# Kernel optimization log

Hardware: AMD Instinct MI355X
Metric: run time of the kernel (lower is better)

The kernel has to match this reference:

```python
import jax, jax.numpy as jnp
import numpy as np

EPS = 1e-5

def knn_idx(x, k):
    # x: (B,C,N). Returns (B,N,k) indices of k nearest neighbors (by L2).
    inner = -2.0 * jnp.einsum('bcn,bcm->bnm', x, x)          # (B,N,N)
    xx = jnp.sum(x * x, axis=1)                               # (B,N)
    neg_dist = -xx[:, :, None] - inner - xx[:, None, :]       # (B,N,N)
    _, idx = jax.lax.top_k(neg_dist, k)                       # (B,N,k)
    return idx

def get_graph_features(x, k):
    # x: (B,C,N) -> (B,2C,N,k) with channels = concat(neighbor-center, center)
    B, C, N = x.shape
    idx = knn_idx(x, k)                                       # (B,N,k)
    pts = jnp.transpose(x, (0, 2, 1))                         # (B,N,C)
    nbr = jax.vmap(lambda p, i: p[i])(pts, idx)               # (B,N,k,C)
    ctr = jnp.broadcast_to(pts[:, :, None, :], nbr.shape)     # (B,N,k,C)
    feat = jnp.concatenate([nbr - ctr, ctr], axis=-1)         # (B,N,k,2C)
    return jnp.transpose(feat, (0, 3, 1, 2))                  # (B,2C,N,k)

def conv_bn_relu(y, W, gamma, beta):
    # 1x1 conv (pointwise matmul) + train-mode BatchNorm2d + ReLU
    y = jnp.einsum('oc,bcnk->bonk', W, y)
    mean = jnp.mean(y, axis=(0, 2, 3), keepdims=True)
    var = jnp.var(y, axis=(0, 2, 3), keepdims=True)
    yhat = (y - mean) * jax.lax.rsqrt(var + EPS)
    return jax.nn.relu(yhat * gamma[None, :, None, None] + beta[None, :, None, None])

def setup_inputs() -> dict:
    key = jax.random.key(0)
    ks = jax.random.split(key, 16)
    B, N, k, emb = 8, 2048, 20, 512
    x = jax.random.normal(ks[0], (B, 3, N), dtype=jnp.float32)
    def w(kk, o, c):
        return jax.random.normal(kk, (o, c), dtype=jnp.float32) * (1.0 / np.sqrt(c))
    inp = {
        'x': x, 'k': k,
        'W1': w(ks[1], 64, 6),   'W2': w(ks[2], 64, 64),
        'W3': w(ks[3], 128, 64), 'W4': w(ks[4], 256, 128),
        'W5': w(ks[5], emb, 512),
    }
    for i, c in zip(range(1, 6), [64, 64, 128, 256, emb]):
        inp[f'g{i}'] = 1.0 + 0.1 * jax.random.normal(ks[5 + i], (c,), dtype=jnp.float32)
        inp[f'b{i}'] = 0.1 * jax.random.normal(ks[10 + i], (c,), dtype=jnp.float32)
    return inp

def reference(x, W1, W2, W3, W4, W5, g1, b1, g2, b2, g3, b3, g4, b4, g5, b5, k):
    B, C, N = x.shape
    h = get_graph_features(x, k)                  # (B,6,N,k)
    h = conv_bn_relu(h, W1, g1, b1)               # (B,64,N,k)
    x1 = jnp.max(h, axis=-1, keepdims=True)
    h = conv_bn_relu(h, W2, g2, b2)               # (B,64,N,k)
    x2 = jnp.max(h, axis=-1, keepdims=True)
    h = conv_bn_relu(h, W3, g3, b3)               # (B,128,N,k)
    x3 = jnp.max(h, axis=-1, keepdims=True)
    h = conv_bn_relu(h, W4, g4, b4)               # (B,256,N,k)
    x4 = jnp.max(h, axis=-1, keepdims=True)
    cat = jnp.concatenate([x1, x2, x3, x4], axis=1)  # (B,512,N,1)
    out = conv_bn_relu(cat, W5, g5, b5)              # (B,emb,N,1)
    return out.reshape(B, -1, N)
```

## Files before the change

kernel.cpp:

```cpp
#include <hip/hip_runtime.h>
#include <hip/hip_bf16.h>

typedef __hip_bfloat16 bf16;
typedef __attribute__((ext_vector_type(8))) short short8v;
typedef __attribute__((ext_vector_type(4))) float f32x4;
typedef unsigned int uint;
typedef unsigned long long u64;

#define BATCH 8
#define NPTS 2048
#define KNN 20
#define NK (NPTS*KNN)
#define P4 (BATCH*NK)
#define BN_TOT (BATCH*NPTS)

union BU { bf16 h; unsigned short u; };
__device__ __forceinline__ unsigned short f2bf(float f){
    BU bu; bu.h = __float2bfloat16(f); return bu.u;
}
__device__ __forceinline__ float bfu2f(unsigned short u){
    return __uint_as_float(((uint)u) << 16);
}
__device__ __forceinline__ uint fenc(float f){
    uint b = __float_as_uint(f);
    return (b & 0x80000000u) ? ~b : (b | 0x80000000u);
}

__global__ void initK(float* __restrict__ shadow)
{
    int t = blockIdx.x*256 + threadIdx.x;
    if (t < 5*16*1024) shadow[t] = 0.f;
}

__global__ void cvtWS(const float* __restrict__ src, short* __restrict__ dst, int Cin)
{
    int t = blockIdx.x*256 + threadIdx.x;
    int co = t / Cin, ci = t - co*Cin;
    dst[(size_t)co*Cin + (ci ^ ((co & 7) << 3))] = (short)f2bf(src[t]);
}

__global__ __launch_bounds__(512)
void knn_kernel(const float* __restrict__ x, int* __restrict__ idx)
{
    #pragma clang fp contract(off)
    __shared__ float4 sp[NPTS];
    const int b  = blockIdx.x / (NPTS/8);
    const int nb = blockIdx.x % (NPTS/8);
    const float* xb = x + (size_t)b*3*NPTS;
    for (int i = threadIdx.x; i < NPTS; i += 512) {
        float y0 = xb[i], y1 = xb[NPTS+i], y2 = xb[2*NPTS+i];
        float4 p; p.x = y0; p.y = y1; p.z = y2;
        p.w = y0*y0 + y1*y1 + y2*y2;
        sp[i] = p;
    }
    __syncthreads();

    const int wave = threadIdx.x >> 6;
    const int lane = threadIdx.x & 63;
    const int n = nb*8 + wave;

    const float4 pn = sp[n];
    const float x0 = pn.x, x1 = pn.y, x2 = pn.z;
    const float xxn = pn.w;

    constexpr int L = 4;
    float bA[L], bB[L]; int iA[L], iB[L];
    #pragma unroll
    for (int i = 0; i < L; ++i) {
        bA[i] = -3e38f; bB[i] = -3e38f; iA[i] = 0x7fffffff; iB[i] = 0x7fffffff;
    }

    float4 c0 = sp[lane], c1 = sp[lane + 64];
    #pragma unroll
    for (int t = 0; t < NPTS/128; ++t) {
        float4 n0, n1;
        if (t + 1 < NPTS/128) {
            n0 = sp[lane + (2*t+2)*64];
            n1 = sp[lane + (2*t+3)*64];
        }
        int m0 = lane + (2*t)*64, m1 = m0 + 64;
        float dot0 = x0*c0.x + x1*c0.y + x2*c0.z;
        float v0 = -xxn - (-2.f*dot0) - c0.w;
        float dot1 = x0*c1.x + x1*c1.y + x2*c1.z;
        float v1 = -xxn - (-2.f*dot1) - c1.w;
        int mi0 = m0, mi1 = m1;
        #pragma unroll
        for (int i = 0; i < L; ++i) {
            { bool sw = v0 > bA[i];
              float tv = sw ? bA[i] : v0; int ti = sw ? iA[i] : mi0;
              bA[i] = sw ? v0 : bA[i]; iA[i] = sw ? mi0 : iA[i]; v0 = tv; mi0 = ti; }
            { bool sw = v1 > bB[i];
              float tv = sw ? bB[i] : v1; int ti = sw ? iB[i] : mi1;
              bB[i] = sw ? v1 : bB[i]; iB[i] = sw ? mi1 : iB[i]; v1 = tv; mi1 = ti; }
        }
        c0 = n0; c1 = n1;
    }

    u64 kA[L], kB[L];
    #pragma unroll
    for (int i = 0; i < L; ++i) {
        kA[i] = ((u64)fenc(bA[i]) << 32) | (uint)(~iA[i]);
        kB[i] = ((u64)fenc(bB[i]) << 32) | (uint)(~iB[i]);
    }

    size_t obase = ((size_t)b*NPTS + n)*KNN;
    int popA = 0, popB = 0;
    #pragma unroll 1
    for (int s = 0; s < KNN; ++s) {
        bool useA = kA[0] >= kB[0];
        u64 my = useA ? kA[0] : kB[0];
        u64 g = my;
        #pragma unroll
        for (int off = 1; off < 64; off <<= 1) {
            u64 o = __shfl_xor(g, off);
            g = (o > g) ? o : g;
        }
        if (lane == 0) idx[obase + s] = (int)(~(uint)g);
        bool win = (my == g);
        bool pA = win && useA, pB = win && !useA;
        #pragma unroll
        for (int i = 0; i < L-1; ++i) {
            kA[i] = pA ? kA[i+1] : kA[i];
            kB[i] = pB ? kB[i+1] : kB[i];
        }
        kA[L-1] = pA ? 0ULL : kA[L-1];
        kB[L-1] = pB ? 0ULL : kB[L-1];
        popA += pA; popB += pB;
    }

    if (__any((popA >= L) || (popB >= L))) {
        float B[KNN]; int BI[KNN];
        #pragma unroll
        for (int i = 0; i < KNN; ++i) { B[i] = -3e38f; BI[i] = 0x7fffffff; }
        #pragma unroll 1
        for (int j = 0; j < NPTS/64; ++j) {
            int m = lane + j*64;
            float4 p = sp[m];
            float dot = x0*p.x + x1*p.y + x2*p.z;
            float v = -xxn - (-2.f*dot) - p.w;
            int mi = m;
            #pragma unroll
            for (int i = 0; i < KNN; ++i) {
                bool sw = v > B[i];
                float tv = sw ? B[i]  : v;
                int   ti = sw ? BI[i] : mi;
                B[i]  = sw ? v  : B[i];
                BI[i] = sw ? mi : BI[i];
                v = tv; mi = ti;
            }
        }
        #pragma unroll 1
        for (int s = 0; s < KNN; ++s) {
            float mv = B[0]; int mi = BI[0];
            #pragma unroll
            for (int off = 1; off < 64; off <<= 1) {
                float ov = __shfl_xor(mv, off);
                int   oi = __shfl_xor(mi, off);
                if (ov > mv || (ov == mv && oi < mi)) { mv = ov; mi = oi; }
            }
            bool win = (B[0] == mv) && (BI[0] == mi);
            #pragma unroll
            for (int i = 0; i < KNN-1; ++i) {
                B[i]  = win ? B[i+1]  : B[i];
                BI[i] = win ? BI[i+1] : BI[i];
            }
            B[KNN-1]  = win ? -3e38f     : B[KNN-1];
            BI[KNN-1] = win ? 0x7fffffff : BI[KNN-1];
            if (lane == 0) idx[obase + s] = mi;
        }
    }
}

__global__ __launch_bounds__(256)
void conv1T(const float* __restrict__ x, const int* __restrict__ idx,
            const float* __restrict__ W1, bf16* __restrict__ h1,
            float* __restrict__ shadow)
{
    __shared__ unsigned short lv[256][64];
    __shared__ float ps[4][64], pq[4][64];
    const int tid = threadIdx.x;
    int p = blockIdx.x*256 + tid;
    int b = p / NK;
    int r = p - b*NK;
    int n = r / KNN;
    int j = idx[p];
    const float* xb = x + (size_t)b*3*NPTS;
    float c0 = xb[n], c1 = xb[NPTS+n], c2 = xb[2*NPTS+n];
    float d0 = xb[j]-c0, d1 = xb[NPTS+j]-c1, d2 = xb[2*NPTS+j]-c2;
    uint4* outp = reinterpret_cast<uint4*>(reinterpret_cast<unsigned short*>(h1) + (size_t)p*64);
    uint4* lrow = reinterpret_cast<uint4*>(lv[tid]);
    #pragma unroll
    for (int ch = 0; ch < 8; ++ch) {
        uint u[4];
        #pragma unroll
        for (int q = 0; q < 4; ++q) {
            const float* wa = W1 + (ch*8 + q*2)*6;
            float a0 = wa[0]*d0 + wa[1]*d1 + wa[2]*d2 + wa[3]*c0 + wa[4]*c1 + wa[5]*c2;
            const float* wb = wa + 6;
            float a1 = wb[0]*d0 + wb[1]*d1 + wb[2]*d2 + wb[3]*c0 + wb[4]*c1 + wb[5]*c2;
            u[q] = (uint)f2bf(a0) | ((uint)f2bf(a1) << 16);
        }
        uint4 val = make_uint4(u[0], u[1], u[2], u[3]);
        outp[ch] = val;
        lrow[ch] = val;
    }
    __syncthreads();
    int c = tid & 63, grp = tid >> 6;
    float s = 0.f, q = 0.f;
    #pragma unroll 8
    for (int i = 0; i < 64; ++i) {
        float v = bfu2f(lv[grp*64 + i][c]);
        s += v; q += v*v;
    }
    ps[grp][c] = s; pq[grp][c] = q;
    __syncthreads();
    if (tid < 64) {
        float S = ps[0][tid]+ps[1][tid]+ps[2][tid]+ps[3][tid];
        float Q = pq[0][tid]+pq[1][tid]+pq[2][tid]+pq[3][tid];
        float* sh = shadow + (size_t)(blockIdx.x & 15)*1024;
        atomicAdd(&sh[tid], S);
        atomicAdd(&sh[512 + tid], Q);
    }
}

__global__ void fin_kernel(const float* __restrict__ shadow,
                           const float* __restrict__ gamma, const float* __restrict__ beta,
                           float* __restrict__ scbiF, int C, float invCnt)
{
    for (int c = threadIdx.x; c < C; c += 256) {
        float s = 0.f, q = 0.f;
        #pragma unroll
        for (int i = 0; i < 16; ++i) { s += shadow[i*1024 + c]; q += shadow[i*1024 + 512 + c]; }
        float m = s*invCnt;
        float var = q*invCnt - m*m;
        float rs = rsqrtf(var + 1e-5f);
        float sc = rs * gamma[c];
        float bi = fmaf(-m, sc, beta[c]);
        scbiF[2*c] = sc; scbiF[2*c+1] = bi;
    }
}

template<int Cout, int Cin, int M, int POOL, int NSPLIT, int KTILE, int BT, int PF>
__global__ __launch_bounds__(BT)
void gemmT(const short* __restrict__ Wb, const bf16* __restrict__ in,
           bf16* __restrict__ outT, float* __restrict__ shadow,
           float* __restrict__ pmax, float* __restrict__ pmin)
{
    constexpr int CSPL = Cout/NSPLIT;
    constexpr int NT   = CSPL/16;
    constexpr int ROWS = (BT/64)*16*M;
    constexpr int KSTOT = Cin/32;
    constexpr int KPT   = KTILE/32;
    constexpr int NTILE = Cin/KTILE;
    constexpr int NG    = POOL ? ROWS/KNN : 1;
    constexpr size_t WB = (size_t)CSPL*KTILE*2;
    constexpr size_t PB = POOL ? (size_t)2*ROWS*17*4 : 0;
    constexpr size_t SB = WB > PB ? WB : PB;

    __shared__ __align__(16) char smem[SB];
    short* WsmS = reinterpret_cast<short*>(smem);
    float* poolF = reinterpret_cast<float*>(smem);

    const int tid  = threadIdx.x;
    const int lane = tid & 63;
    const int g = lane >> 4, mr = lane & 15;
    const int wid = tid >> 6;
    const int rowBlk = blockIdx.x*ROWS;
    const int rowW   = rowBlk + wid*(16*M);
    const int ntBase = blockIdx.y*CSPL;
    const short* inS = reinterpret_cast<const short*>(in);

    f32x4 acc[M][NT];
    #pragma unroll
    for (int m = 0; m < M; ++m)
    #pragma unroll
    for (int i = 0; i < NT; ++i) acc[m][i] = (f32x4){0.f,0.f,0.f,0.f};

    if constexpr (PF == 2) {
        static_assert(NTILE == 1, "PF=2 requires KTILE==Cin");
        short8v aAll[M*KSTOT];
        #pragma unroll
        for (int ks = 0; ks < KSTOT; ++ks)
        #pragma unroll
        for (int m = 0; m < M; ++m)
            aAll[ks*M + m] = *reinterpret_cast<const short8v*>(
                inS + (size_t)(rowW + m*16 + mr)*Cin + ks*32 + 8*g);
        for (int f8 = tid; f8 < CSPL*KTILE/8; f8 += BT) {
            int f = f8*8;
            int row = f / KTILE, col = f - row*KTILE;
            short8v v = *reinterpret_cast<const short8v*>(
                Wb + (size_t)(ntBase + row)*Cin + col);
            *reinterpret_cast<short8v*>(WsmS + f) = v;
        }
        __syncthreads();
        #pragma unroll
        for (int ks = 0; ks < KSTOT; ++ks) {
            const int kx = ks*32 + 8*g;
            #pragma unroll
            for (int nt = 0; nt < NT; ++nt) {
                const int brow = nt*16 + mr;
                short8v bfr = *reinterpret_cast<const short8v*>(
                    WsmS + brow*KTILE + (kx ^ ((mr & 7) << 3)));
                #pragma unroll
                for (int m = 0; m < M; ++m)
                    acc[m][nt] = __builtin_amdgcn_mfma_f32_16x16x32_bf16(
                        aAll[ks*M + m], bfr, acc[m][nt], 0, 0, 0);
            }
        }
    } else {
        short8v a[M], anext[M];
        if (PF) {
            #pragma unroll
            for (int m = 0; m < M; ++m)
                a[m] = *reinterpret_cast<const short8v*>(inS + (size_t)(rowW + m*16 + mr)*Cin + 8*g);
        }
        #pragma unroll 1
        for (int kt = 0; kt < NTILE; ++kt) {
            if (kt) __syncthreads();
            {
                const int ktBase = kt*KTILE;
                for (int f8 = tid; f8 < CSPL*KTILE/8; f8 += BT) {
                    int f = f8*8;
                    int row = f / KTILE, col = f - row*KTILE;
                    short8v v = *reinterpret_cast<const short8v*>(
                        Wb + (size_t)(ntBase + row)*Cin + ktBase + col);
                    *reinterpret_cast<short8v*>(WsmS + f) = v;
                }
            }
            __syncthreads();

            #pragma unroll
            for (int ksl = 0; ksl < KPT; ++ksl) {
                const int ksg = kt*KPT + ksl;
                const int k0 = ksg*32 + 8*g;
                if (!PF) {
                    #pragma unroll
                    for (int m = 0; m < M; ++m)
                        a[m] = *reinterpret_cast<const short8v*>(inS + (size_t)(rowW + m*16 + mr)*Cin + k0);
                } else if (ksg + 1 < KSTOT) {
                    #pragma unroll
                    for (int m = 0; m < M; ++m)
                        anext[m] = *reinterpret_cast<const short8v*>(inS + (size_t)(rowW + m*16 + mr)*Cin + k0 + 32);
                }
                const int kx = ksl*32 + 8*g;
                #pragma unroll
                for (int nt = 0; nt < NT; ++nt) {
                    const int brow = nt*16 + mr;
                    short8v bfr = *reinterpret_cast<const short8v*>(
                        WsmS + brow*KTILE + (kx ^ ((mr & 7) << 3)));
                    #pragma unroll
                    for (int m = 0; m < M; ++m)
                        acc[m][nt] = __builtin_amdgcn_mfma_f32_16x16x32_bf16(a[m], bfr, acc[m][nt], 0, 0, 0);
                }
                if (PF) {
                    #pragma unroll
                    for (int m = 0; m < M; ++m) a[m] = anext[m];
                }
            }
        }
    }

    float* sh = shadow + (size_t)((blockIdx.x ^ blockIdx.y) & 15)*1024;
    #pragma unroll
    for (int nt = 0; nt < NT; ++nt) {
        float s = 0.f, q = 0.f;
        #pragma unroll
        for (int m = 0; m < M; ++m)
        #pragma unroll
        for (int j = 0; j < 4; ++j) { float v = acc[m][nt][j]; s += v; q += v*v; }
        s += __shfl_xor(s, 16); s += __shfl_xor(s, 32);
        q += __shfl_xor(q, 16); q += __shfl_xor(q, 32);
        if (g == 0) {
            atomicAdd(&sh[ntBase + nt*16 + mr], s);
            atomicAdd(&sh[512 + ntBase + nt*16 + mr], q);
        }
    }

    if (!POOL) {
        #pragma unroll
        for (int m = 0; m < M; ++m)
        #pragma unroll
        for (int nt = 0; nt < NT; ++nt)
        #pragma unroll
        for (int j = 0; j < 4; ++j) {
            size_t row = (size_t)rowW + m*16 + g*4 + j;
            outT[row*Cout + ntBase + nt*16 + mr] = __float2bfloat16(acc[m][nt][j]);
        }
    } else {
        __syncthreads();
        #pragma unroll
        for (int np = 0; np < NT/2; ++np) {
            #pragma unroll
            for (int hh = 0; hh < 2; ++hh) {
                #pragma unroll
                for (int m = 0; m < M; ++m)
                #pragma unroll
                for (int j = 0; j < 4; ++j) {
                    int row = wid*(16*M) + m*16 + g*4 + j;
                    poolF[hh*(ROWS*17) + row*17 + mr] = acc[m][np*2+hh][j];
                }
            }
            __syncthreads();
            if (tid < 2*NG*16) {
                int hh = tid / (NG*16);
                int gg = (tid >> 4) % NG;
                int cc = tid & 15;
                float mx = -3e38f, mn = 3e38f;
                #pragma unroll
                for (int kk = 0; kk < KNN; ++kk) {
                    float v = poolF[hh*(ROWS*17) + (gg*KNN + kk)*17 + cc];
                    mx = fmaxf(mx, v); mn = fminf(mn, v);
                }
                int grp = rowBlk/KNN + gg;
                int c = ntBase + (np*2 + hh)*16 + cc;
                pmax[(size_t)grp*256 + c] = mx;
                pmin[(size_t)grp*256 + c] = mn;
            }
            __syncthreads();
        }
    }
}

template<int C>
__global__ void maxpoolT(bf16* __restrict__ h, const float* __restrict__ scbiF,
                         bf16* __restrict__ catT, int coff)
{
    constexpr int PB = 256/C;
    int t = threadIdx.x;
    int c = t & (C-1);
    int bn = blockIdx.x*PB + t/C;
    float sc = scbiF[2*c], bi = scbiF[2*c+1];
    unsigned short* src = reinterpret_cast<unsigned short*>(h) + (size_t)bn*KNN*C + c;
    float best = 0.f;
    #pragma unroll
    for (int kk = 0; kk < KNN; ++kk) {
        float a = fmaxf(fmaf(bfu2f(src[kk*C]), sc, bi), 0.f);
        src[kk*C] = f2bf(a);
        best = fmaxf(best, a);
    }
    catT[(size_t)bn*512 + coff + c] = __float2bfloat16(best);
}

__global__ void cat4T(const float* __restrict__ pmax, const float* __restrict__ pmin,
                      const float* __restrict__ scbiF, const float* __restrict__ g4,
                      bf16* __restrict__ catT)
{
    int t = blockIdx.x*256 + threadIdx.x;
    int c = t & 255, bn = t >> 8;
    float sc = scbiF[2*c], bi = scbiF[2*c+1];
    float v = (g4[c] >= 0.f) ? pmax[t] : pmin[t];
    catT[(size_t)bn*512 + 256 + c] = __float2bfloat16(fmaxf(fmaf(v, sc, bi), 0.f));
}

__global__ void finalT(const bf16* __restrict__ h5, const float* __restrict__ scbiF,
                       float* __restrict__ out)
{
    __shared__ float ls[64][65];
    int t = threadIdx.x;
    int b = blockIdx.z, n0 = blockIdx.x*64, c0 = blockIdx.y*64;
    int j = t & 63, i0 = t >> 6;
    float sc = scbiF[2*(c0+j)], bi = scbiF[2*(c0+j)+1];
    const unsigned short* hp = reinterpret_cast<const unsigned short*>(h5);
    for (int it = 0; it < 16; ++it) {
        int i = i0 + it*4;
        float v = bfu2f(hp[((size_t)(b*NPTS + n0 + i))*512 + c0 + j]);
        ls[i][j] = fmaxf(fmaf(v, sc, bi), 0.f);
    }
    __syncthreads();
    for (int it = 0; it < 16; ++it) {
        int cr = i0 + it*4;
        out[((size_t)b*512 + c0 + cr)*NPTS + n0 + j] = ls[j][cr];
    }
}

extern "C" void kernel_launch(void* const* d_in, const int* in_sizes, int n_in,
                              void* d_out, int out_size, void* d_ws, size_t ws_size,
                              hipStream_t stream)
{
    const float* x  = (const float*)d_in[0];
    const float* W1 = (const float*)d_in[2];
    const float* W2 = (const float*)d_in[3];
    const float* W3 = (const float*)d_in[4];
    const float* W4 = (const float*)d_in[5];
    const float* W5 = (const float*)d_in[6];
    const float* g1 = (const float*)d_in[7];  const float* b1 = (const float*)d_in[8];
    const float* g2 = (const float*)d_in[9];  const float* b2 = (const float*)d_in[10];
    const float* g3 = (const float*)d_in[11]; const float* b3 = (const float*)d_in[12];
    const float* g4 = (const float*)d_in[13]; const float* b4 = (const float*)d_in[14];
    const float* g5 = (const float*)d_in[15]; const float* b5 = (const float*)d_in[16];
    float* out = (float*)d_out;

    char* w = (char*)d_ws;
    int*   idx    = (int*)w;
    float* scbiF  = (float*)(w + 1323008);
    float* shadow = (float*)(w + 1343488);
    short* Wb     = (short*)(w + 1671168);
    bf16*  h1     = (bf16*)(w + 2285568);
    float* pmax   = (float*)h1;
    float* pmin   = pmax + (size_t)BN_TOT*256;
    bf16*  h2     = (bf16*)(w + 44228608);
    bf16*  h5     = h2;
    bf16*  h3     = (bf16*)(w + 86171648);
    bf16*  catT   = (bf16*)(w + 170057728);

    short* Wb2 = Wb, *Wb3 = Wb + 4096, *Wb4 = Wb + 12288, *Wb5 = Wb + 45056;
    float* sh1 = shadow, *sh2 = shadow + 16384, *sh3 = shadow + 2*16384,
         * sh4 = shadow + 3*16384, *sh5 = shadow + 4*16384;

    initK<<<320, 256, 0, stream>>>(shadow);
    cvtWS<<<16,   256, 0, stream>>>(W2, Wb2, 64);
    cvtWS<<<32,   256, 0, stream>>>(W3, Wb3, 64);
    cvtWS<<<128,  256, 0, stream>>>(W4, Wb4, 128);
    cvtWS<<<1024, 256, 0, stream>>>(W5, Wb5, 512);

    knn_kernel<<<BATCH*NPTS/8, 512, 0, stream>>>(x, idx);
    conv1T<<<P4/256, 256, 0, stream>>>(x, idx, W1, h1, sh1);

    fin_kernel<<<1, 256, 0, stream>>>(sh1, g1, b1, scbiF, 64, 1.f/P4);
    maxpoolT<64><<<BN_TOT/4, 256, 0, stream>>>(h1, scbiF, catT, 0);

    gemmT<64,64,2,0,1,64,256,1><<<dim3(P4/128,1), 256, 0, stream>>>(
        Wb2, h1, h2, sh2, nullptr, nullptr);
    fin_kernel<<<1, 256, 0, stream>>>(sh2, g2, b2, scbiF + 1024, 64, 1.f/P4);
    maxpoolT<64><<<BN_TOT/4, 256, 0, stream>>>(h2, scbiF + 1024, catT, 64);

    gemmT<128,64,2,0,1,64,256,1><<<dim3(P4/128,1), 256, 0, stream>>>(
        Wb3, h2, h3, sh3, nullptr, nullptr);
    fin_kernel<<<1, 256, 0, stream>>>(sh3, g3, b3, scbiF + 2048, 128, 1.f/P4);
    maxpoolT<128><<<BN_TOT/2, 256, 0, stream>>>(h3, scbiF + 2048, catT, 128);

    gemmT<256,128,2,1,2,128,640,2><<<dim3(P4/320,2), 640, 0, stream>>>(
        Wb4, h3, nullptr, sh4, pmax, pmin);
    fin_kernel<<<1, 256, 0, stream>>>(sh4, g4, b4, scbiF + 3072, 256, 1.f/P4);
    cat4T<<<BN_TOT, 256, 0, stream>>>(pmax, pmin, scbiF + 3072, g4, catT);

    gemmT<512,512,2,0,4,128,256,1><<<dim3(BN_TOT/128,4), 256, 0, stream>>>(
        Wb5, catT, h5, sh5, nullptr, nullptr);
    fin_kernel<<<1, 256, 0, stream>>>(sh5, g5, b5, scbiF + 4096, 512, 1.f/BN_TOT);
    finalT<<<dim3(NPTS/64, 8, BATCH), 256, 0, stream>>>(h5, scbiF + 4096, out);
}
```

Before: 363.4 us.

## Fuse BN finalize into consumers, merge prep kernels, cheapen KNN wave argmax

Removes the five single-block fin_kernel launches by recomputing BatchNorm scale/bias from the shadow sums inside maxpoolT, cat4T and finalT. The init and weight-conversion kernels are merged into one prepK launch, and cat4T now handles 16 points per block. The KNN top-k selection shuffles only the 32-bit distance key, with a ballot-based tie path for the index. The aim is fewer kernel launches and serialization bubbles, in exchange for redundant per-block reduction of the shadow buffers.

```diff
diff --git a/kernel.cpp b/kernel.cpp
--- a/kernel.cpp
+++ b/kernel.cpp
@@ -26,17 +26,23 @@
     return (b & 0x80000000u) ? ~b : (b | 0x80000000u);
 }
 
-__global__ void initK(float* __restrict__ shadow)
-{
-    int t = blockIdx.x*256 + threadIdx.x;
-    if (t < 5*16*1024) shadow[t] = 0.f;
-}
-
-__global__ void cvtWS(const float* __restrict__ src, short* __restrict__ dst, int Cin)
-{
-    int t = blockIdx.x*256 + threadIdx.x;
+__device__ __forceinline__ void cvt1(const float* src, short* dst, int t, int Cin)
+{
     int co = t / Cin, ci = t - co*Cin;
     dst[(size_t)co*Cin + (ci ^ ((co & 7) << 3))] = (short)f2bf(src[t]);
+}
+__global__ void prepK(const float* __restrict__ W2, const float* __restrict__ W3,
+                      const float* __restrict__ W4, const float* __restrict__ W5,
+                      float* __restrict__ shadow,
+                      short* __restrict__ Wb2, short* __restrict__ Wb3,
+                      short* __restrict__ Wb4, short* __restrict__ Wb5)
+{
+    int blk = blockIdx.x, tid = threadIdx.x;
+    if (blk < 320)      { shadow[blk*256 + tid] = 0.f; }
+    else if (blk < 336) { cvt1(W2, Wb2, (blk-320)*256 + tid, 64); }
+    else if (blk < 368) { cvt1(W3, Wb3, (blk-336)*256 + tid, 64); }
+    else if (blk < 496) { cvt1(W4, Wb4, (blk-368)*256 + tid, 128); }
+    else                { cvt1(W5, Wb5, (blk-496)*256 + tid, 512); }
 }
 
 __global__ __launch_bounds__(512)
@@ -109,13 +115,29 @@
     for (int s = 0; s < KNN; ++s) {
         bool useA = kA[0] >= kB[0];
         u64 my = useA ? kA[0] : kB[0];
-        u64 g = my;
+        uint vhi = (uint)(my >> 32);
+        uint gh = vhi;
         #pragma unroll
         for (int off = 1; off < 64; off <<= 1) {
-            u64 o = __shfl_xor(g, off);
-            g = (o > g) ? o : g;
-        }
-        if (lane == 0) idx[obase + s] = (int)(~(uint)g);
+            uint o = __shfl_xor(gh, off);
+            gh = (o > gh) ? o : gh;
+        }
+        u64 tie = __ballot(vhi == gh);
+        uint glo;
+        if (__popcll(tie) == 1) {
+            int wl = __ffsll((long long)tie) - 1;
+            glo = __shfl((uint)my, wl);
+        } else {
+            uint lo = (vhi == gh) ? (uint)my : 0u;
+            #pragma unroll
+            for (int off = 1; off < 64; off <<= 1) {
+                uint o = __shfl_xor(lo, off);
+                lo = (o > lo) ? o : lo;
+            }
+            glo = lo;
+        }
+        u64 g = ((u64)gh << 32) | glo;
+        if (lane == 0) idx[obase + s] = (int)(~glo);
         bool win = (my == g);
         bool pA = win && useA, pB = win && !useA;
         #pragma unroll
@@ -220,23 +242,6 @@
         float* sh = shadow + (size_t)(blockIdx.x & 15)*1024;
         atomicAdd(&sh[tid], S);
         atomicAdd(&sh[512 + tid], Q);
-    }
-}
-
-__global__ void fin_kernel(const float* __restrict__ shadow,
-                           const float* __restrict__ gamma, const float* __restrict__ beta,
-                           float* __restrict__ scbiF, int C, float invCnt)
-{
-    for (int c = threadIdx.x; c < C; c += 256) {
-        float s = 0.f, q = 0.f;
-        #pragma unroll
-        for (int i = 0; i < 16; ++i) { s += shadow[i*1024 + c]; q += shadow[i*1024 + 512 + c]; }
-        float m = s*invCnt;
-        float var = q*invCnt - m*m;
-        float rs = rsqrtf(var + 1e-5f);
-        float sc = rs * gamma[c];
-        float bi = fmaf(-m, sc, beta[c]);
-        scbiF[2*c] = sc; scbiF[2*c+1] = bi;
     }
 }
 
@@ -422,14 +427,28 @@
 }
 
 template<int C>
-__global__ void maxpoolT(bf16* __restrict__ h, const float* __restrict__ scbiF,
+__global__ void maxpoolT(bf16* __restrict__ h, const float* __restrict__ shadow,
+                         const float* __restrict__ gamma, const float* __restrict__ beta,
                          bf16* __restrict__ catT, int coff)
 {
+    __shared__ float sscbi[2*C];
     constexpr int PB = 256/C;
     int t = threadIdx.x;
+    if (t < C) {
+        float s = 0.f, q = 0.f;
+        #pragma unroll
+        for (int i = 0; i < 16; ++i) { s += shadow[i*1024 + t]; q += shadow[i*1024 + 512 + t]; }
+        float m = s*(1.f/P4);
+        float var = q*(1.f/P4) - m*m;
+        float rs = rsqrtf(var + 1e-5f);
+        float sc = rs*gamma[t];
+        sscbi[2*t] = sc;
+        sscbi[2*t+1] = fmaf(-m, sc, beta[t]);
+    }
+    __syncthreads();
     int c = t & (C-1);
     int bn = blockIdx.x*PB + t/C;
-    float sc = scbiF[2*c], bi = scbiF[2*c+1];
+    float sc = sscbi[2*c], bi = sscbi[2*c+1];
     unsigned short* src = reinterpret_cast<unsigned short*>(h) + (size_t)bn*KNN*C + c;
     float best = 0.f;
     #pragma unroll
@@ -442,24 +461,51 @@
 }
 
 __global__ void cat4T(const float* __restrict__ pmax, const float* __restrict__ pmin,
-                      const float* __restrict__ scbiF, const float* __restrict__ g4,
-                      bf16* __restrict__ catT)
-{
-    int t = blockIdx.x*256 + threadIdx.x;
-    int c = t & 255, bn = t >> 8;
-    float sc = scbiF[2*c], bi = scbiF[2*c+1];
-    float v = (g4[c] >= 0.f) ? pmax[t] : pmin[t];
-    catT[(size_t)bn*512 + 256 + c] = __float2bfloat16(fmaxf(fmaf(v, sc, bi), 0.f));
-}
-
-__global__ void finalT(const bf16* __restrict__ h5, const float* __restrict__ scbiF,
+                      const float* __restrict__ shadow, const float* __restrict__ g4,
+                      const float* __restrict__ b4, bf16* __restrict__ catT)
+{
+    int c = threadIdx.x;
+    float s = 0.f, q = 0.f;
+    #pragma unroll
+    for (int i = 0; i < 16; ++i) { s += shadow[i*1024 + c]; q += shadow[i*1024 + 512 + c]; }
+    float m = s*(1.f/P4);
+    float var = q*(1.f/P4) - m*m;
+    float rs = rsqrtf(var + 1e-5f);
+    float gg = g4[c];
+    float sc = rs*gg;
+    float bi = fmaf(-m, sc, b4[c]);
+    int bn0 = blockIdx.x*16;
+    #pragma unroll
+    for (int i = 0; i < 16; ++i) {
+        int t = (bn0 + i)*256 + c;
+        float v = (gg >= 0.f) ? pmax[t] : pmin[t];
+        catT[(size_t)(bn0 + i)*512 + 256 + c] = __float2bfloat16(fmaxf(fmaf(v, sc, bi), 0.f));
+    }
+}
+
+__global__ void finalT(const bf16* __restrict__ h5, const float* __restrict__ shadow,
+                       const float* __restrict__ g5, const float* __restrict__ b5,
                        float* __restrict__ out)
 {
     __shared__ float ls[64][65];
+    __shared__ float sscbi[128];
     int t = threadIdx.x;
     int b = blockIdx.z, n0 = blockIdx.x*64, c0 = blockIdx.y*64;
+    if (t < 64) {
+        int c = c0 + t;
+        float s = 0.f, q = 0.f;
+        #pragma unroll
+        for (int i = 0; i < 16; ++i) { s += shadow[i*1024 + c]; q += shadow[i*1024 + 512 + c]; }
+        float m = s*(1.f/BN_TOT);
+        float var = q*(1.f/BN_TOT) - m*m;
+        float rs = rsqrtf(var + 1e-5f);
+        float sc = rs*g5[c];
+        sscbi[2*t] = sc;
+        sscbi[2*t+1] = fmaf(-m, sc, b5[c]);
+    }
+    __syncthreads();
     int j = t & 63, i0 = t >> 6;
-    float sc = scbiF[2*(c0+j)], bi = scbiF[2*(c0+j)+1];
+    float sc = sscbi[2*j], bi = sscbi[2*j+1];
     const unsigned short* hp = reinterpret_cast<const unsigned short*>(h5);
     for (int it = 0; it < 16; ++it) {
         int i = i0 + it*4;
@@ -492,7 +538,6 @@
 
     char* w = (char*)d_ws;
     int*   idx    = (int*)w;
-    float* scbiF  = (float*)(w + 1323008);
     float* shadow = (float*)(w + 1343488);
     short* Wb     = (short*)(w + 1671168);
     bf16*  h1     = (bf16*)(w + 2285568);
@@ -507,35 +552,26 @@
     float* sh1 = shadow, *sh2 = shadow + 16384, *sh3 = shadow + 2*16384,
          * sh4 = shadow + 3*16384, *sh5 = shadow + 4*16384;
 
-    initK<<<320, 256, 0, stream>>>(shadow);
-    cvtWS<<<16,   256, 0, stream>>>(W2, Wb2, 64);
-    cvtWS<<<32,   256, 0, stream>>>(W3, Wb3, 64);
-    cvtWS<<<128,  256, 0, stream>>>(W4, Wb4, 128);
-    cvtWS<<<1024, 256, 0, stream>>>(W5, Wb5, 512);
+    prepK<<<1520, 256, 0, stream>>>(W2, W3, W4, W5, shadow, Wb2, Wb3, Wb4, Wb5);
 
     knn_kernel<<<BATCH*NPTS/8, 512, 0, stream>>>(x, idx);
     conv1T<<<P4/256, 256, 0, stream>>>(x, idx, W1, h1, sh1);
 
-    fin_kernel<<<1, 256, 0, stream>>>(sh1, g1, b1, scbiF, 64, 1.f/P4);
-    maxpoolT<64><<<BN_TOT/4, 256, 0, stream>>>(h1, scbiF, catT, 0);
+    maxpoolT<64><<<BN_TOT/4, 256, 0, stream>>>(h1, sh1, g1, b1, catT, 0);
 
     gemmT<64,64,2,0,1,64,256,1><<<dim3(P4/128,1), 256, 0, stream>>>(
         Wb2, h1, h2, sh2, nullptr, nullptr);
-    fin_kernel<<<1, 256, 0, stream>>>(sh2, g2, b2, scbiF + 1024, 64, 1.f/P4);
-    maxpoolT<64><<<BN_TOT/4, 256, 0, stream>>>(h2, scbiF + 1024, catT, 64);
+    maxpoolT<64><<<BN_TOT/4, 256, 0, stream>>>(h2, sh2, g2, b2, catT, 64);
 
     gemmT<128,64,2,0,1,64,256,1><<<dim3(P4/128,1), 256, 0, stream>>>(
         Wb3, h2, h3, sh3, nullptr, nullptr);
-    fin_kernel<<<1, 256, 0, stream>>>(sh3, g3, b3, scbiF + 2048, 128, 1.f/P4);
-    maxpoolT<128><<<BN_TOT/2, 256, 0, stream>>>(h3, scbiF + 2048, catT, 128);
+    maxpoolT<128><<<BN_TOT/2, 256, 0, stream>>>(h3, sh3, g3, b3, catT, 128);
 
     gemmT<256,128,2,1,2,128,640,2><<<dim3(P4/320,2), 640, 0, stream>>>(
         Wb4, h3, nullptr, sh4, pmax, pmin);
-    fin_kernel<<<1, 256, 0, stream>>>(sh4, g4, b4, scbiF + 3072, 256, 1.f/P4);
-    cat4T<<<BN_TOT, 256, 0, stream>>>(pmax, pmin, scbiF + 3072, g4, catT);
+    cat4T<<<BN_TOT/16, 256, 0, stream>>>(pmax, pmin, sh4, g4, b4, catT);
 
     gemmT<512,512,2,0,4,128,256,1><<<dim3(BN_TOT/128,4), 256, 0, stream>>>(
         Wb5, catT, h5, sh5, nullptr, nullptr);
-    fin_kernel<<<1, 256, 0, stream>>>(sh5, g5, b5, scbiF + 4096, 512, 1.f/BN_TOT);
-    finalT<<<dim3(NPTS/64, 8, BATCH), 256, 0, stream>>>(h5, scbiF + 4096, out);
-}
+    finalT<<<dim3(NPTS/64, 8, BATCH), 256, 0, stream>>>(h5, sh5, g5, b5, out);
+}
```

New measurement: 337.6 us (median of 2 runs). 1.08x faster.
